# Performance work log

Measured on AMD Instinct MI355X. Metric: run time of the kernel, lower is better.

## Reference

```python
import jax, jax.numpy as jnp
import numpy as np
import math

FACTOR = 5

def setup_inputs() -> dict:
    key = jax.random.key(0)
    k1, k2, k3, k4 = jax.random.split(key, 4)
    B, L, H, D = 2, 4096, 8, 64
    sample_k = min(FACTOR * int(np.ceil(np.log(L))), L)  # 45
    return {
        "queries": jax.random.normal(k1, (B, L, H, D), dtype=jnp.float32),
        "keys": jax.random.normal(k2, (B, L, H, D), dtype=jnp.float32),
        "values": jax.random.normal(k3, (B, L, H, D), dtype=jnp.float32),
        "attn_mask": jnp.zeros((1,), dtype=bool),  # unused (mask_flag=False)
        "index_sample": jax.random.randint(k4, (L, sample_k), 0, L, dtype=jnp.int64),
    }

def reference(queries, keys, values, attn_mask, index_sample):
    B, L_Q, H, D = queries.shape
    L_K = keys.shape[1]
    # [B,L,H,D] -> [B,H,L,D]
    q = jnp.transpose(queries, (0, 2, 1, 3))
    k = jnp.transpose(keys, (0, 2, 1, 3))
    v = jnp.transpose(values, (0, 2, 1, 3))

    n_top = min(FACTOR * int(np.ceil(np.log(L_Q))), L_Q)  # u

    # --- _prob_QK ---
    # K_sample[b,h,l,s,e] = k[b,h,index_sample[l,s],e]
    K_sample = k[:, :, index_sample, :]                      # [B,H,L_Q,S,E]
    Q_K_sample = jnp.einsum('bhle,bhlse->bhls', q, K_sample)  # [B,H,L_Q,S]
    # sparsity measure: max - mean(over full L_K as in torch code)
    M = Q_K_sample.max(axis=-1) - Q_K_sample.sum(axis=-1) / L_K  # [B,H,L_Q]
    M_top = jax.lax.top_k(M, n_top)[1]                        # [B,H,u] indices

    Q_reduce = jnp.take_along_axis(q, M_top[..., None], axis=2)  # [B,H,u,E]
    scores_top = jnp.einsum('bhue,bhke->bhuk', Q_reduce, k)      # [B,H,u,L_K]

    scale = 1.0 / math.sqrt(D)
    attn = jax.nn.softmax(scale * scores_top, axis=-1)           # [B,H,u,L_K]
    context_in_q = jnp.einsum('bhuk,bhkd->bhud', attn, v)        # [B,H,u,D]

    # scatter selected contexts into zero-initialized tensor
    b_idx = jnp.arange(B)[:, None, None]
    h_idx = jnp.arange(H)[None, :, None]
    context = jnp.zeros((B, H, L_Q, D), dtype=queries.dtype)
    context = context.at[b_idx, h_idx, M_top].set(context_in_q)

    return jnp.transpose(context, (0, 2, 1, 3))  # [B,L_Q,H,D]
```

## Files before the change

kernel.cpp:

```cpp
#include <hip/hip_runtime.h>
#include <math.h>

#define B_ 2
#define L_ 4096
#define H_ 8
#define D_ 64
#define S_ 45
#define NTOP_ 45
#define SCALE 0.125f
#define TKEYS 64
#define NSPLIT 64

__global__ __launch_bounds__(256) void compute_M_kernel(
    const float* __restrict__ q, const float* __restrict__ k,
    const int* __restrict__ samp, float* __restrict__ M) {
    __shared__ int sIdx[32 * 48];
    int tid = threadIdx.x;
    int g   = blockIdx.x;
    int xcd = g & 7;
    int s0  = g >> 3;
    int bh  = xcd + 8 * (s0 >> 7);
    int c32 = s0 & 127;
    int b = bh >> 3, h = bh & 7;
    int l0 = c32 * 32;

    const int* sbase = samp + (long)l0 * S_;
    for (int i = tid; i < 32 * S_; i += 256) {
        int qq = i / S_, ss = i - qq * S_;
        sIdx[qq * 48 + ss] = sbase[i];
    }
    if (tid < 96) sIdx[(tid >> 2) * 48 + S_ + (tid & 3) % 3] = 0;
    __syncthreads();

    int lane = tid & 63, wave = tid >> 6;
    int l8 = lane & 7;
    int q8 = lane >> 3;
    int qi = wave * 8 + q8;
    int l  = l0 + qi;

    const float4* qrow = (const float4*)(q + (((long)(b * L_ + l)) * H_ + h) * D_);
    float4 qa = qrow[l8], qb = qrow[8 + l8];

    const float4* kb4 = (const float4*)(k + ((long)b * L_ * H_ + h) * (long)D_);
    const int* myIdx = sIdx + qi * 48;

    const float4* r0 = kb4 + (long)myIdx[0] * (H_ * D_ / 4);
    float4 ka0 = r0[l8], kb0 = r0[8 + l8];
    const float4* r1 = kb4 + (long)myIdx[1] * (H_ * D_ / 4);
    float4 ka1 = r1[l8], kb1 = r1[8 + l8];

    float vmax = -INFINITY, vsum = 0.f;
    #pragma unroll 3
    for (int s = 0; s < S_; ++s) {
        int nidx = myIdx[s + 2];
        const float4* nr = kb4 + (long)nidx * (H_ * D_ / 4);
        float4 na = nr[l8], nb = nr[8 + l8];

        float p = qa.x * ka0.x + qa.y * ka0.y + qa.z * ka0.z + qa.w * ka0.w
                + qb.x * kb0.x + qb.y * kb0.y + qb.z * kb0.z + qb.w * kb0.w;
        p += __shfl_xor(p, 1, 64);
        p += __shfl_xor(p, 2, 64);
        p += __shfl_xor(p, 4, 64);
        vmax = fmaxf(vmax, p);
        vsum += p;

        ka0 = ka1; kb0 = kb1;
        ka1 = na;  kb1 = nb;
    }
    if (l8 == 0) M[(long)bh * L_ + l] = vmax - vsum * (1.0f / (float)L_);
}

__global__ __launch_bounds__(256) void topk_kernel(
    const float* __restrict__ M, int* __restrict__ topIdx) {
    __shared__ unsigned int hist[256];
    __shared__ unsigned int suf[257];
    __shared__ unsigned int wsum[4];
    __shared__ int sBin, sRemain, sCnt, sTieCnt;
    __shared__ int tie[64];

    int bh = blockIdx.x, tid = threadIdx.x;
    int lane = tid & 63, wave = tid >> 6;
    const float* row = M + (long)bh * L_;

    unsigned int key[16];
    #pragma unroll
    for (int j = 0; j < 16; ++j) {
        unsigned int bts = __float_as_uint(row[tid + 256 * j]);
        key[j] = bts ^ ((unsigned int)((int)bts >> 31) | 0x80000000u);
    }

    unsigned int prefix = 0, pmask = 0;
    int remain = NTOP_;
    #pragma unroll 1
    for (int pass = 3; pass >= 0; --pass) {
        int shift = pass * 8;
        hist[tid] = 0;
        __syncthreads();
        #pragma unroll
        for (int j = 0; j < 16; ++j) {
            if ((key[j] & pmask) == prefix)
                atomicAdd(&hist[(key[j] >> shift) & 255u], 1u);
        }
        __syncthreads();
        unsigned int s = hist[tid];
        #pragma unroll
        for (int off = 1; off < 64; off <<= 1) {
            unsigned int o = __shfl_down(s, off, 64);
            if (lane + off < 64) s += o;
        }
        if (lane == 0) wsum[wave] = s;
        __syncthreads();
        unsigned int add = 0;
        for (int w = wave + 1; w < 4; ++w) add += wsum[w];
        s += add;
        suf[tid] = s;
        if (tid == 0) suf[256] = 0;
        __syncthreads();
        if (suf[tid] >= (unsigned int)remain && suf[tid + 1] < (unsigned int)remain) {
            sBin = tid;
            sRemain = remain - (int)suf[tid + 1];
        }
        __syncthreads();
        prefix |= ((unsigned int)sBin) << shift;
        pmask  |= 0xFFu << shift;
        remain  = sRemain;
        __syncthreads();
    }

    if (tid == 0) { sCnt = 0; sTieCnt = 0; }
    __syncthreads();
    int* outRow = topIdx + bh * NTOP_;
    #pragma unroll
    for (int j = 0; j < 16; ++j) {
        int idx = tid + 256 * j;
        if (key[j] > prefix) {
            int pos = atomicAdd(&sCnt, 1);
            outRow[pos] = idx;
        } else if (key[j] == prefix) {
            int tp = atomicAdd(&sTieCnt, 1);
            if (tp < 64) tie[tp] = idx;
        }
    }
    __syncthreads();
    if (tid == 0) {
        int base = sCnt;
        int tc = sTieCnt < 64 ? sTieCnt : 64;
        for (int t = 0; t < remain; ++t) {
            int mi = 0x7fffffff, mj = 0;
            for (int j2 = 0; j2 < tc; ++j2)
                if (tie[j2] < mi) { mi = tie[j2]; mj = j2; }
            outRow[base + t] = mi;
            tie[mj] = 0x7fffffff;
        }
    }
}

#define STRIDE 68
__global__ __launch_bounds__(256, 2) void attn_strip_kernel(
    const float* __restrict__ q, const float* __restrict__ k,
    const float* __restrict__ v, const int* __restrict__ topIdx,
    float* __restrict__ pOut, float* __restrict__ plPart, int nsplit) {
    __shared__ float sQ[48 * STRIDE];
    __shared__ float sK[TKEYS * STRIDE];
    __shared__ float sV[TKEYS * STRIDE];
    __shared__ float sP[48 * STRIDE];

    int g = blockIdx.x;
    int xcd = g & 7;
    int s0 = g >> 3;
    int grp = s0 / nsplit;
    int bh = xcd + 8 * grp;
    int split = s0 - grp * nsplit;
    int b = bh >> 3, h = bh & 7;
    int tid = threadIdx.x;
    int key0 = split * TKEYS;

    #pragma unroll
    for (int j = 0; j < 3; ++j) {
        int i = tid + 256 * j;
        int u = i >> 4, d4 = i & 15;
        float4 val = make_float4(0.f, 0.f, 0.f, 0.f);
        if (u < NTOP_) {
            int lq = topIdx[bh * NTOP_ + u];
            val = *(const float4*)(q + (((long)(b * L_ + lq)) * H_ + h) * D_ + 4 * d4);
        }
        *(float4*)(sQ + u * STRIDE + 4 * d4) = val;
    }
    #pragma unroll
    for (int j = 0; j < 4; ++j) {
        int i = tid + 256 * j;
        int r = i >> 4, d4 = i & 15;
        long off = (((long)(b * L_ + key0 + r)) * H_ + h) * D_ + 4 * d4;
        *(float4*)(sK + r * STRIDE + 4 * d4) = *(const float4*)(k + off);
        *(float4*)(sV + r * STRIDE + 4 * d4) = *(const float4*)(v + off);
    }
    __syncthreads();

    int tx = tid & 15, ty = tid >> 4;
    float acc[3][4];
    #pragma unroll
    for (int i = 0; i < 3; ++i)
        #pragma unroll
        for (int j = 0; j < 4; ++j) acc[i][j] = 0.f;

    #pragma unroll 4
    for (int d4 = 0; d4 < 16; ++d4) {
        float4 qv[3];
        #pragma unroll
        for (int i = 0; i < 3; ++i)
            qv[i] = *(const float4*)(sQ + (3 * ty + i) * STRIDE + 4 * d4);
        #pragma unroll
        for (int j = 0; j < 4; ++j) {
            float4 kv = *(const float4*)(sK + (tx + 16 * j) * STRIDE + 4 * d4);
            #pragma unroll
            for (int i = 0; i < 3; ++i)
                acc[i][j] += qv[i].x * kv.x + qv[i].y * kv.y + qv[i].z * kv.z + qv[i].w * kv.w;
        }
    }
    #pragma unroll
    for (int i = 0; i < 3; ++i) {
        #pragma unroll
        for (int j = 0; j < 4; ++j)
            sP[(3 * ty + i) * STRIDE + tx + 16 * j] = __expf(acc[i][j] * SCALE);
    }
    __syncthreads();

    int dx = tid & 15, uy = tid >> 4;
    float o[3][4];
    float ls[3];
    #pragma unroll
    for (int i = 0; i < 3; ++i) {
        ls[i] = 0.f;
        #pragma unroll
        for (int c = 0; c < 4; ++c) o[i][c] = 0.f;
    }
    #pragma unroll 4
    for (int k4 = 0; k4 < 16; ++k4) {
        float pa[3][4];
        #pragma unroll
        for (int i = 0; i < 3; ++i)
            *(float4*)pa[i] = *(const float4*)(sP + (3 * uy + i) * STRIDE + 4 * k4);
        #pragma unroll
        for (int c = 0; c < 4; ++c) {
            float4 vr = *(const float4*)(sV + (4 * k4 + c) * STRIDE + 4 * dx);
            #pragma unroll
            for (int i = 0; i < 3; ++i) {
                o[i][0] += pa[i][c] * vr.x;
                o[i][1] += pa[i][c] * vr.y;
                o[i][2] += pa[i][c] * vr.z;
                o[i][3] += pa[i][c] * vr.w;
                ls[i]   += pa[i][c];
            }
        }
    }
    #pragma unroll
    for (int i = 0; i < 3; ++i) {
        int u = 3 * uy + i;
        if (u < NTOP_) {
            long base = ((long)(split * 16 + bh) * NTOP_ + u) * D_;
            *(float4*)(pOut + base + 4 * dx) = make_float4(o[i][0], o[i][1], o[i][2], o[i][3]);
            if (dx == 0) plPart[(long)(split * 16 + bh) * NTOP_ + u] = ls[i];
        }
    }
}

__global__ __launch_bounds__(256) void reduce_norm_kernel(
    const int* __restrict__ topIdx, const float* __restrict__ pOut,
    const float* __restrict__ plPart, float* __restrict__ out, int nsplit) {
    __shared__ float part[4][64];
    __shared__ float lpart[4];
    int u = blockIdx.x, bh = blockIdx.y;
    int b = bh >> 3, h = bh & 7;
    int tid = threadIdx.x;
    int d = tid & 63, sg = tid >> 6;
    float acc = 0.f, lsum = 0.f;
    for (int s = sg; s < nsplit; s += 4) {
        acc  += pOut[((long)(s * 16 + bh) * NTOP_ + u) * D_ + d];
        lsum += plPart[(long)(s * 16 + bh) * NTOP_ + u];
    }
    part[sg][d] = acc;
    if (d == 0) lpart[sg] = lsum;
    __syncthreads();
    if (sg == 0) {
        float a = part[0][d] + part[1][d] + part[2][d] + part[3][d];
        float lt = lpart[0] + lpart[1] + lpart[2] + lpart[3];
        int lq = topIdx[bh * NTOP_ + u];
        out[(((long)(b * L_ + lq)) * H_ + h) * D_ + d] = a / lt;
    }
}

extern "C" void kernel_launch(void* const* d_in, const int* in_sizes, int n_in,
                              void* d_out, int out_size, void* d_ws, size_t ws_size,
                              hipStream_t stream) {
    const float* q = (const float*)d_in[0];
    const float* k = (const float*)d_in[1];
    const float* v = (const float*)d_in[2];
    const int* samp = (const int*)d_in[4];
    float* out = (float*)d_out;

    char* ws = (char*)d_ws;
    const size_t mBytes   = (size_t)B_ * H_ * L_ * sizeof(float);
    const size_t topBytes = (size_t)B_ * H_ * NTOP_ * sizeof(int);
    const size_t plBytes  = (size_t)NSPLIT * 16 * NTOP_ * sizeof(float);
    float* M      = (float*)ws;
    int*   topIdx = (int*)(ws + mBytes);
    float* plPart = (float*)(ws + mBytes + topBytes);
    float* pOut   = (float*)(ws + mBytes + topBytes + plBytes);

    int nsplit = NSPLIT;
    while (nsplit > 1) {
        size_t need = mBytes + topBytes + plBytes +
                      (size_t)nsplit * 16 * NTOP_ * D_ * sizeof(float);
        if (need <= ws_size) break;
        nsplit >>= 1;
    }

    hipMemsetAsync(d_out, 0, (size_t)out_size * sizeof(float), stream);

    compute_M_kernel<<<2048, 256, 0, stream>>>(q, k, samp, M);

    topk_kernel<<<B_ * H_, 256, 0, stream>>>(M, topIdx);

    attn_strip_kernel<<<nsplit * B_ * H_, 256, 0, stream>>>(
        q, k, v, topIdx, pOut, plPart, nsplit);

    dim3 gn(NTOP_, B_ * H_);
    reduce_norm_kernel<<<gn, 256, 0, stream>>>(topIdx, pOut, plPart, out, nsplit);
}
```

Baseline: 158.9 us.

## Restructure M computation so each wave gathers full key rows across all heads

The sparsity-measure kernel now gives each wave one query position and covers all eight heads at once, instead of one head for 32 queries. Each lane reads eight contiguous floats, so every sampled key row is fetched as one contiguous 2KB span. The sample indices, which depend only on the position and not the head, are loaded once and shared across heads. The aim is better coalescing and fewer separate narrow gathers, at the cost of per-head L2 locality, since heads are no longer pinned to XCDs.

```diff
diff --git a/kernel.cpp b/kernel.cpp
--- a/kernel.cpp
+++ b/kernel.cpp
@@ -14,47 +14,43 @@
 __global__ __launch_bounds__(256) void compute_M_kernel(
     const float* __restrict__ q, const float* __restrict__ k,
     const int* __restrict__ samp, float* __restrict__ M) {
-    __shared__ int sIdx[32 * 48];
+    __shared__ int sIdx[4 * 48];
     int tid = threadIdx.x;
     int g   = blockIdx.x;
     int xcd = g & 7;
     int s0  = g >> 3;
-    int bh  = xcd + 8 * (s0 >> 7);
-    int c32 = s0 & 127;
-    int b = bh >> 3, h = bh & 7;
-    int l0 = c32 * 32;
-
-    const int* sbase = samp + (long)l0 * S_;
-    for (int i = tid; i < 32 * S_; i += 256) {
-        int qq = i / S_, ss = i - qq * S_;
-        sIdx[qq * 48 + ss] = sbase[i];
-    }
-    if (tid < 96) sIdx[(tid >> 2) * 48 + S_ + (tid & 3) % 3] = 0;
-    __syncthreads();
-
-    int lane = tid & 63, wave = tid >> 6;
-    int l8 = lane & 7;
-    int q8 = lane >> 3;
-    int qi = wave * 8 + q8;
-    int l  = l0 + qi;
-
-    const float4* qrow = (const float4*)(q + (((long)(b * L_ + l)) * H_ + h) * D_);
-    float4 qa = qrow[l8], qb = qrow[8 + l8];
-
-    const float4* kb4 = (const float4*)(k + ((long)b * L_ * H_ + h) * (long)D_);
-    const int* myIdx = sIdx + qi * 48;
+    int b   = xcd >> 2;
+    int chunk = (xcd & 3) + 4 * s0;
+    int l0  = chunk * 4;
+
+    if (tid < 4 * S_) {
+        int qq = tid / S_, ss = tid - qq * S_;
+        sIdx[qq * 48 + ss] = samp[(long)(l0 + qq) * S_ + ss];
+    }
+    if (tid < 12) sIdx[(tid / 3) * 48 + S_ + (tid % 3)] = 0;
+    __syncthreads();
+
+    int lane = tid & 63, w = tid >> 6;
+    int l = l0 + w;
+    int h = lane >> 3, part = lane & 7;
+
+    const float4* qrow = (const float4*)(q + ((long)(b * L_ + l)) * (H_ * D_));
+    float4 qa = qrow[2 * lane], qb = qrow[2 * lane + 1];
+
+    const float4* kb4 = (const float4*)(k + (long)b * L_ * (H_ * D_));
+    const int* myIdx = sIdx + w * 48;
 
     const float4* r0 = kb4 + (long)myIdx[0] * (H_ * D_ / 4);
-    float4 ka0 = r0[l8], kb0 = r0[8 + l8];
+    float4 ka0 = r0[2 * lane], kb0 = r0[2 * lane + 1];
     const float4* r1 = kb4 + (long)myIdx[1] * (H_ * D_ / 4);
-    float4 ka1 = r1[l8], kb1 = r1[8 + l8];
+    float4 ka1 = r1[2 * lane], kb1 = r1[2 * lane + 1];
 
     float vmax = -INFINITY, vsum = 0.f;
     #pragma unroll 3
     for (int s = 0; s < S_; ++s) {
         int nidx = myIdx[s + 2];
         const float4* nr = kb4 + (long)nidx * (H_ * D_ / 4);
-        float4 na = nr[l8], nb = nr[8 + l8];
+        float4 na = nr[2 * lane], nb = nr[2 * lane + 1];
 
         float p = qa.x * ka0.x + qa.y * ka0.y + qa.z * ka0.z + qa.w * ka0.w
                 + qb.x * kb0.x + qb.y * kb0.y + qb.z * kb0.z + qb.w * kb0.w;
@@ -67,7 +63,8 @@
         ka0 = ka1; kb0 = kb1;
         ka1 = na;  kb1 = nb;
     }
-    if (l8 == 0) M[(long)bh * L_ + l] = vmax - vsum * (1.0f / (float)L_);
+    if (part == 0)
+        M[((long)(b * H_ + h)) * L_ + l] = vmax - vsum * (1.0f / (float)L_);
 }
 
 __global__ __launch_bounds__(256) void topk_kernel(
```

Measured after the change: 184.8 us. +16.3%, slower.
